# Optimization experiments

Measured on AMD Instinct MI355X. Metric: run time of the kernel, lower is better.

The kernel has to match this reference:

```python
import jax, jax.numpy as jnp
import numpy as np

N = 100000      # num_nodes
E = 1600000     # num_edges (avg degree 16)
D_IN = 128
D_H = 128
D_OUT = 128


def setup_inputs() -> dict:
    key = jax.random.key(0)
    ks = jax.random.split(key, 6)
    x = jax.random.normal(ks[0], (N, D_IN), dtype=jnp.float32)
    edge_index = jax.random.randint(ks[1], (2, E), 0, N, dtype=jnp.int32)
    s_in = 1.0 / np.sqrt(D_IN)
    s_h = 1.0 / np.sqrt(D_H)
    # nn.Linear weights have shape [out_features, in_features]
    w_neigh1 = jax.random.uniform(ks[2], (D_H, D_IN), jnp.float32, -s_in, s_in)
    w_root1 = jax.random.uniform(ks[3], (D_H, D_IN), jnp.float32, -s_in, s_in)
    w_neigh2 = jax.random.uniform(ks[4], (D_OUT, D_H), jnp.float32, -s_h, s_h)
    w_root2 = jax.random.uniform(ks[5], (D_OUT, D_H), jnp.float32, -s_h, s_h)
    return {
        "x": x,
        "w_neigh1": w_neigh1,
        "w_root1": w_root1,
        "w_neigh2": w_neigh2,
        "w_root2": w_root2,
        "edge_index": edge_index,
    }


def reference(x, w_neigh1, w_root1, w_neigh2, w_root2, edge_index):
    row = edge_index[0]  # destination (row of adjacency)
    col = edge_index[1]  # source / neighbor (column of adjacency)
    # row-normalized adjacency: adj[row, col] = 1 / deg(row)
    deg = jax.ops.segment_sum(jnp.ones(E, x.dtype), row, num_segments=N)
    inv_deg = jnp.where(deg > 0, 1.0 / jnp.maximum(deg, 1.0), 0.0)  # [N]

    def mean_agg(h):
        # spmm: gather neighbor feats [E, d], scatter-add to rows, normalize
        return jax.ops.segment_sum(h[col], row, num_segments=N) * inv_deg[:, None]

    # layer 0: relu(adj @ x @ Wn1^T + x @ Wr1^T)
    h = jax.nn.relu(mean_agg(x) @ w_neigh1.T + x @ w_root1.T)
    # layer 1: adj @ h @ Wn2^T + h @ Wr2^T
    return mean_agg(h) @ w_neigh2.T + h @ w_root2.T
```

## Files before the change

### kernel.cpp

```cpp
#include <hip/hip_runtime.h>

#define NBUK_MAX 2048
#define BNODE 64
#define BCAP 2048
#define AGG_NODES 16
#define AGG_CAP 768
#define SUPER_SHIFT 11
#define NSUPER_MAX 64
#define SCAP 65536
#define SUB_PER_SUPER 32

#define QSCALE (127.0f / 6.0f)
#define DEQ (6.0f / 127.0f)

typedef __attribute__((ext_vector_type(8))) short bf16x8;
typedef __attribute__((ext_vector_type(4))) float f32x4;

static __device__ __forceinline__ unsigned int f2bf(float f) {
  unsigned int t = __builtin_bit_cast(unsigned int, f);
  t += 0x7fff + ((t >> 16) & 1);
  return t >> 16;
}
static __device__ __forceinline__ unsigned char f2q(float v) {
  float q = rintf(v * QSCALE);
  q = fminf(fmaxf(q, -127.f), 127.f);
  return (unsigned char)(signed char)(int)q;
}



__global__ __launch_bounds__(256) void zero_kernel(int* __restrict__ p, int n) {
  int i = blockIdx.x * 256 + threadIdx.x;
  if (i < n) p[i] = 0;
}


__global__ __launch_bounds__(256) void prep_kernel(
    const float* __restrict__ x, unsigned short* __restrict__ Xp,
    unsigned char* __restrict__ Xq, const float* __restrict__ wn1,
    const float* __restrict__ wr1, const float* __restrict__ wn2,
    const float* __restrict__ wr2, unsigned short* __restrict__ Wp, int N,
    int cvtB) {
  const int b = blockIdx.x;
  const int tid = threadIdx.x;
  if (b < cvtB) {
    int i = b * 256 + tid;
    int n4 = N * 32;
    if (i < n4) {
      float4 v = ((const float4*)x)[i];
      unsigned int oq = (unsigned)f2q(v.x) | ((unsigned)f2q(v.y) << 8) |
                        ((unsigned)f2q(v.z) << 16) | ((unsigned)f2q(v.w) << 24);
      ((unsigned int*)Xq)[i] = oq;
      int r = i >> 5;
      int f0 = (i & 31) << 2;
      int tile = r >> 6, w = (r >> 4) & 3, m = r & 15;
      int ks = f0 >> 5, kgrp = (f0 >> 3) & 3, j0 = f0 & 7;
      unsigned dst =
          (unsigned)tile * 8192 + w * 2048 + ks * 512 + (kgrp * 16 + m) * 8 + j0;
      uint2 o;
      o.x = f2bf(v.x) | (f2bf(v.y) << 16);
      o.y = f2bf(v.z) | (f2bf(v.w) << 16);
      *(uint2*)(Xp + dst) = o;
    }
  } else {
    int i = (b - cvtB) * 256 + tid;
    int layer = i >> 15;
    int r = i & 32767;
    int ks = r >> 12;
    int nf = (r >> 9) & 7;
    int lane = (r >> 3) & 63;
    int j = r & 7;
    const float* src = layer ? ((ks < 4) ? wn2 : wr2) : ((ks < 4) ? wn1 : wr1);
    int m = lane & 15, kgrp = lane >> 4;
    int kk = (ks & 3) * 32 + kgrp * 8 + j;
    int n = nf * 16 + m;
    Wp[i] = (unsigned short)f2bf(src[n * 128 + kk]);
  }
}


__global__ __launch_bounds__(256) void s1_scatter(
    const int* __restrict__ row, const int* __restrict__ col,
    int* __restrict__ sfill, int* __restrict__ sbuf, int E) {
  __shared__ int cnt[NSUPER_MAX];
  __shared__ int base[NSUPER_MAX];
  int per = (E + gridDim.x - 1) / gridDim.x;
  int e0 = blockIdx.x * per;
  int e1 = e0 + per;
  if (e1 > E) e1 = E;
  if (threadIdx.x < NSUPER_MAX) cnt[threadIdx.x] = 0;
  __syncthreads();
  for (int e = e0 + threadIdx.x; e < e1; e += 256)
    atomicAdd(&cnt[row[e] >> SUPER_SHIFT], 1);
  __syncthreads();
  if (threadIdx.x < NSUPER_MAX) {
    int c = cnt[threadIdx.x];
    base[threadIdx.x] =
        c ? (threadIdx.x * SCAP + atomicAdd(&sfill[threadIdx.x], c)) : 0;
    cnt[threadIdx.x] = 0;
  }
  __syncthreads();
  for (int e = e0 + threadIdx.x; e < e1; e += 256) {
    int r = row[e];
    int sp = r >> SUPER_SHIFT;
    int rk = atomicAdd(&cnt[sp], 1);
    int w = base[sp] + rk;
    if (w < (sp + 1) * SCAP)
      sbuf[w] = ((r & ((1 << SUPER_SHIFT) - 1)) << 17) | col[e];
  }
}


__global__ __launch_bounds__(256) void s2_scatter(
    const int* __restrict__ sfillr, const int* __restrict__ sbuf,
    int* __restrict__ bfill, int* __restrict__ bbuf, int nbuk) {
  __shared__ int cnt[SUB_PER_SUPER];
  __shared__ int base[SUB_PER_SUPER];
  const int sp = blockIdx.x >> 4;
  const int bp = blockIdx.x & 15;
  const int b0 = sp * SUB_PER_SUPER;
  int scnt = sfillr[sp];
  if (scnt > SCAP) scnt = SCAP;
  const int sbase = sp * SCAP;
  const int i0 = sbase + (scnt * bp) / 16;
  const int i1 = sbase + (scnt * (bp + 1)) / 16;
  if (threadIdx.x < SUB_PER_SUPER) cnt[threadIdx.x] = 0;
  __syncthreads();
  for (int i = i0 + threadIdx.x; i < i1; i += 256)
    atomicAdd(&cnt[(((unsigned)sbuf[i]) >> 17) >> 6], 1);
  __syncthreads();
  if (threadIdx.x < SUB_PER_SUPER) {
    int c = cnt[threadIdx.x];
    int b = b0 + threadIdx.x;
    base[threadIdx.x] = c ? (b * BCAP + atomicAdd(&bfill[b], c)) : 0;
    cnt[threadIdx.x] = 0;
  }
  __syncthreads();
  for (int i = i0 + threadIdx.x; i < i1; i += 256) {
    int p = sbuf[i];
    unsigned rl = ((unsigned)p) >> 17;
    int sub = rl >> 6;
    int rk = atomicAdd(&cnt[sub], 1);
    int w = base[sub] + rk;
    if (w < (b0 + sub + 1) * BCAP)
      bbuf[w] = ((rl & 63) << 17) | (p & 0x1FFFF);
  }
}


__global__ __launch_bounds__(256) void p2_sort_kernel(
    const int* __restrict__ bfillr, int* __restrict__ bbuf,
    int* __restrict__ rowptr, int* __restrict__ bsz, int N) {
  __shared__ int cols[BCAP];
  __shared__ int hist[BNODE], startc[BNODE], fillc[BNODE];
  const int b = blockIdx.x;
  const int tid = threadIdx.x;
  const int gs = b * BCAP;
  int bsize = bfillr[b];
  if (bsize > BCAP) bsize = BCAP;
  if (tid < BNODE) hist[tid] = 0;
  __syncthreads();
  for (int i = tid; i < bsize; i += 256)
    atomicAdd(&hist[((unsigned)bbuf[gs + i]) >> 17], 1);
  __syncthreads();
  if (tid < 64) {
    int v = hist[tid];
    int s = v;
    #pragma unroll
    for (int off = 1; off < 64; off <<= 1) {
      int u = __shfl_up(s, off, 64);
      if (tid >= off) s += u;
    }
    startc[tid] = s - v;
    fillc[tid] = s - v;
  }
  __syncthreads();
  for (int i = tid; i < bsize; i += 256) {
    int p = bbuf[gs + i];
    int k = atomicAdd(&fillc[((unsigned)p) >> 17], 1);
    cols[k] = p & 0x1FFFF;
  }
  __syncthreads();
  for (int i = tid; i < bsize; i += 256) bbuf[gs + i] = cols[i];
  if (tid < BNODE) {
    int node = b * BNODE + tid;
    if (node <= N) rowptr[node] = gs + startc[tid];
  }
  if (tid == 0) bsz[b] = bsize;
}


__global__ __launch_bounds__(256) void agg_i8_kernel(
    const unsigned char* __restrict__ qtab, const int* __restrict__ rowptr,
    const int* __restrict__ bbuf, const int* __restrict__ bsz,
    unsigned short* __restrict__ outp, int N) {
  __shared__ int cols[AGG_CAP];
  __shared__ int rp[AGG_NODES + 1];
  const int tid = threadIdx.x;
  const int n0 = blockIdx.x * AGG_NODES;
  const int b = n0 >> 6;
  if (tid <= AGG_NODES) {
    int nn = n0 + tid;
    if (tid == AGG_NODES && (nn & 63) == 0) {
      rp[tid] = b * BCAP + bsz[b];
    } else {
      rp[tid] = rowptr[nn > N ? N : nn];
    }
  }
  __syncthreads();
  const int e0 = rp[0];
  const int range = rp[AGG_NODES] - e0;
  const bool lds = (range <= AGG_CAP);
  if (lds) {
    for (int i = tid; i < range; i += 256) cols[i] = bbuf[e0 + i];
  }
  __syncthreads();

  const int g = tid >> 4;
  const int fl = tid & 15;
  const int node = n0 + g;
  if (node >= N) return;
  const int d = rp[g + 1] - rp[g];
  const char* fb = (const char*)qtab;
  const unsigned foff = (unsigned)fl * 8;
  int a[8];
  #pragma unroll
  for (int j = 0; j < 8; ++j) a[j] = 0;

  const int* cp = lds ? (cols + (rp[g] - e0)) : (bbuf + rp[g]);
  for (int k0 = 0; k0 < d; k0 += 96) {
    int kend = d < k0 + 96 ? d : k0 + 96;
    unsigned sLoX = 0, sHiX = 0, sLoY = 0, sHiY = 0;
    int k = k0;
    for (; k + 8 <= kend; k += 8) {
      unsigned o[8];
      #pragma unroll
      for (int j = 0; j < 8; ++j) o[j] = ((unsigned)cp[k + j] << 7) + foff;
      uint2 v[8];
      #pragma unroll
      for (int j = 0; j < 8; ++j) v[j] = *(const uint2*)(fb + o[j]);
      #pragma unroll
      for (int j = 0; j < 8; ++j) {
        unsigned ux = v[j].x ^ 0x80808080u;
        unsigned uy = v[j].y ^ 0x80808080u;
        sLoX += ux & 0x00FF00FFu;
        sHiX += (ux >> 8) & 0x00FF00FFu;
        sLoY += uy & 0x00FF00FFu;
        sHiY += (uy >> 8) & 0x00FF00FFu;
      }
    }
    for (; k < kend; ++k) {
      uint2 v = *(const uint2*)(fb + (((unsigned)cp[k] << 7) + foff));
      unsigned ux = v.x ^ 0x80808080u;
      unsigned uy = v.y ^ 0x80808080u;
      sLoX += ux & 0x00FF00FFu;
      sHiX += (ux >> 8) & 0x00FF00FFu;
      sLoY += uy & 0x00FF00FFu;
      sHiY += (uy >> 8) & 0x00FF00FFu;
    }
    a[0] += (int)(sLoX & 0xFFFFu);
    a[2] += (int)(sLoX >> 16);
    a[1] += (int)(sHiX & 0xFFFFu);
    a[3] += (int)(sHiX >> 16);
    a[4] += (int)(sLoY & 0xFFFFu);
    a[6] += (int)(sLoY >> 16);
    a[5] += (int)(sHiY & 0xFFFFu);
    a[7] += (int)(sHiY >> 16);
  }
  const int bias = 128 * d;
  #pragma unroll
  for (int j = 0; j < 8; ++j) a[j] -= bias;

  float m = ((d > 0) ? 1.0f / (float)d : 0.f) * DEQ;
  uint4 pk;
  pk.x = f2bf((float)a[0] * m) | (f2bf((float)a[1] * m) << 16);
  pk.y = f2bf((float)a[2] * m) | (f2bf((float)a[3] * m) << 16);
  pk.z = f2bf((float)a[4] * m) | (f2bf((float)a[5] * m) << 16);
  pk.w = f2bf((float)a[6] * m) | (f2bf((float)a[7] * m) << 16);
  unsigned dst = ((unsigned)(node >> 6)) * 8192 + (((node >> 4) & 3) * 2048) +
                 ((fl >> 2) * 512) + (((fl & 3) * 16 + (node & 15)) * 8);
  *(uint4*)(outp + dst) = pk;
}


template <bool L1>
__global__ __launch_bounds__(256) void mfma_gemm_kernel(
    const unsigned short* __restrict__ Aagg_p,
    const unsigned short* __restrict__ Aroot_p,
    const unsigned short* __restrict__ Wpack,
    unsigned short* __restrict__ Hp, unsigned char* __restrict__ Hq,
    float* __restrict__ Cf, int nrows) {
  const int tid = threadIdx.x;
  const int lane = tid & 63;
  const int wid = tid >> 6;
  const int tile = blockIdx.x;
  const int n0 = tile * 64;
  const unsigned abase = (unsigned)tile * 8192 + wid * 2048 + lane * 8;

  bf16x8 a[8];
  #pragma unroll
  for (int ks = 0; ks < 4; ++ks)
    a[ks] = *(const bf16x8*)(Aagg_p + abase + ks * 512);
  #pragma unroll
  for (int ks = 0; ks < 4; ++ks)
    a[4 + ks] = *(const bf16x8*)(Aroot_p + abase + ks * 512);

  f32x4 acc[8];
  #pragma unroll
  for (int i = 0; i < 8; ++i) acc[i] = (f32x4){0.f, 0.f, 0.f, 0.f};
  const unsigned short* wp = Wpack + (size_t)lane * 8;
  #pragma unroll
  for (int ks = 0; ks < 8; ++ks) {
    #pragma unroll
    for (int nf = 0; nf < 8; ++nf) {
      bf16x8 bfr = *(const bf16x8*)(wp + ((ks * 8 + nf) << 9));
      acc[nf] = __builtin_amdgcn_mfma_f32_16x16x32_bf16(a[ks], bfr, acc[nf], 0, 0, 0);
    }
  }

  const int m = lane & 15;
  const int kgrp = lane >> 4;
  const int crow0 = n0 + (wid << 4) + kgrp * 4;
  #pragma unroll
  for (int nf = 0; nf < 8; ++nf) {
    int c = nf * 16 + m;
    #pragma unroll
    for (int j = 0; j < 4; ++j) {
      int r = crow0 + j;
      if (r < nrows) {
        float v = acc[nf][j];
        if (L1) {
          v = fmaxf(v, 0.f);
          unsigned dst = (unsigned)tile * 8192 + wid * 2048 + (c >> 5) * 512 +
                         ((((c >> 3) & 3) * 16) + (kgrp * 4 + j)) * 8 + (c & 7);
          Hp[dst] = (unsigned short)f2bf(v);
          Hq[(size_t)r * 128 + c] = f2q(v);
        } else {
          Cf[(size_t)r * 128 + c] = v;
        }
      }
    }
  }
}


extern "C" void kernel_launch(void* const* d_in, const int* in_sizes, int n_in,
                              void* d_out, int out_size, void* d_ws, size_t ws_size,
                              hipStream_t stream) {
  const float* x = (const float*)d_in[0];
  const float* wn1 = (const float*)d_in[1];
  const float* wr1 = (const float*)d_in[2];
  const float* wn2 = (const float*)d_in[3];
  const float* wr2 = (const float*)d_in[4];
  const int* ei = (const int*)d_in[5];
  const int N = in_sizes[0] / 128;
  const int E = in_sizes[5] / 2;
  const int* row = ei;
  const int* col = ei + E;
  const int NBUK = (N + BNODE - 1) / BNODE;
  const int NSUPER = (N + (1 << SUPER_SHIFT) - 1) >> SUPER_SHIFT;
  const size_t NT = (size_t)(N + 63) / 64;

  char* p = (char*)d_ws;
  unsigned short* Xp = (unsigned short*)p;  p += NT * 8192 * 2;
  unsigned short* Hp = (unsigned short*)p;  p += NT * 8192 * 2;
  unsigned short* Ap = (unsigned short*)p;  p += NT * 8192 * 2;
  unsigned char* Xq = (unsigned char*)p;    p += (size_t)N * 128;
  unsigned char* Hq = (unsigned char*)p;    p += (size_t)N * 128;
  int* sbuf = (int*)p;      p += (size_t)NSUPER_MAX * SCAP * 4;
  int* bbuf = (int*)p;      p += (size_t)NBUK_MAX * BCAP * 4;
  int* rowptr = (int*)p;    p += (size_t)(N + 1) * 4;
  int* sfill = (int*)p;     p += NSUPER_MAX * 4;
  int* bfill = (int*)p;     p += NBUK_MAX * 4;
  int* bsz = (int*)p;       p += NBUK_MAX * 4;
  unsigned short* Wp = (unsigned short*)p;  p += 2 * 32768 * 2;
  unsigned short* Wp1 = Wp;
  unsigned short* Wp2 = Wp + 32768;
  unsigned short* A2p = Xp;

  zero_kernel<<<(NSUPER_MAX + NBUK_MAX + 255) / 256, 256, 0, stream>>>(
      sfill, NSUPER_MAX + NBUK_MAX);

  int cvtB = (N * 32 + 255) / 256;
  prep_kernel<<<cvtB + 256, 256, 0, stream>>>(x, Xp, Xq, wn1, wr1, wn2, wr2, Wp,
                                              N, cvtB);

  s1_scatter<<<512, 256, 0, stream>>>(row, col, sfill, sbuf, E);
  s2_scatter<<<NSUPER * 16, 256, 0, stream>>>(sfill, sbuf, bfill, bbuf, NBUK);
  p2_sort_kernel<<<NBUK, 256, 0, stream>>>(bfill, bbuf, rowptr, bsz, N);

  agg_i8_kernel<<<(N + AGG_NODES - 1) / AGG_NODES, 256, 0, stream>>>(
      Xq, rowptr, bbuf, bsz, Ap, N);
  mfma_gemm_kernel<true><<<(int)NT, 256, 0, stream>>>(Ap, Xp, Wp1, Hp, Hq,
                                                      nullptr, N);

  agg_i8_kernel<<<(N + AGG_NODES - 1) / AGG_NODES, 256, 0, stream>>>(
      Hq, rowptr, bbuf, bsz, A2p, N);
  mfma_gemm_kernel<false><<<(int)NT, 256, 0, stream>>>(A2p, Hp, Wp2, nullptr,
                                                       nullptr, (float*)d_out, N);
}
```

Baseline: 179.3 us.

## Fuse edge scatter into prep kernel and split neighbor lists across lanes

The first-stage edge scatter now runs as extra blocks inside the input/weight conversion kernel, which removes one launch and lets the two independent jobs overlap. The int8 aggregation kernel now gives each 64-lane wavefront four nodes in turn. The four 16-lane slots split each node's neighbor list, and the partial sums are combined with cross-lane shuffles. This is meant to cut per-thread serial latency on long neighbor lists and balance load across degrees, at the cost of shuffle reductions and idle slots on low-degree nodes.

```diff
diff --git a/kernel.cpp b/kernel.cpp
--- a/kernel.cpp
+++ b/kernel.cpp
@@ -9,6 +9,7 @@
 #define NSUPER_MAX 64
 #define SCAP 65536
 #define SUB_PER_SUPER 32
+#define S1_BLOCKS 512
 
 #define QSCALE (127.0f / 6.0f)
 #define DEQ (6.0f / 127.0f)
@@ -39,8 +40,11 @@
     const float* __restrict__ x, unsigned short* __restrict__ Xp,
     unsigned char* __restrict__ Xq, const float* __restrict__ wn1,
     const float* __restrict__ wr1, const float* __restrict__ wn2,
-    const float* __restrict__ wr2, unsigned short* __restrict__ Wp, int N,
-    int cvtB) {
+    const float* __restrict__ wr2, unsigned short* __restrict__ Wp,
+    const int* __restrict__ row, const int* __restrict__ col,
+    int* __restrict__ sfill, int* __restrict__ sbuf, int N, int E, int cvtB) {
+  __shared__ int cnt[NSUPER_MAX];
+  __shared__ int base[NSUPER_MAX];
   const int b = blockIdx.x;
   const int tid = threadIdx.x;
   if (b < cvtB) {
@@ -62,7 +66,7 @@
       o.y = f2bf(v.z) | (f2bf(v.w) << 16);
       *(uint2*)(Xp + dst) = o;
     }
-  } else {
+  } else if (b < cvtB + 256) {
     int i = (b - cvtB) * 256 + tid;
     int layer = i >> 15;
     int r = i & 32767;
@@ -75,38 +79,31 @@
     int kk = (ks & 3) * 32 + kgrp * 8 + j;
     int n = nf * 16 + m;
     Wp[i] = (unsigned short)f2bf(src[n * 128 + kk]);
-  }
-}
-
-
-__global__ __launch_bounds__(256) void s1_scatter(
-    const int* __restrict__ row, const int* __restrict__ col,
-    int* __restrict__ sfill, int* __restrict__ sbuf, int E) {
-  __shared__ int cnt[NSUPER_MAX];
-  __shared__ int base[NSUPER_MAX];
-  int per = (E + gridDim.x - 1) / gridDim.x;
-  int e0 = blockIdx.x * per;
-  int e1 = e0 + per;
-  if (e1 > E) e1 = E;
-  if (threadIdx.x < NSUPER_MAX) cnt[threadIdx.x] = 0;
-  __syncthreads();
-  for (int e = e0 + threadIdx.x; e < e1; e += 256)
-    atomicAdd(&cnt[row[e] >> SUPER_SHIFT], 1);
-  __syncthreads();
-  if (threadIdx.x < NSUPER_MAX) {
-    int c = cnt[threadIdx.x];
-    base[threadIdx.x] =
-        c ? (threadIdx.x * SCAP + atomicAdd(&sfill[threadIdx.x], c)) : 0;
-    cnt[threadIdx.x] = 0;
-  }
-  __syncthreads();
-  for (int e = e0 + threadIdx.x; e < e1; e += 256) {
-    int r = row[e];
-    int sp = r >> SUPER_SHIFT;
-    int rk = atomicAdd(&cnt[sp], 1);
-    int w = base[sp] + rk;
-    if (w < (sp + 1) * SCAP)
-      sbuf[w] = ((r & ((1 << SUPER_SHIFT) - 1)) << 17) | col[e];
+  } else {
+    int hb = b - cvtB - 256;
+    int per = (E + S1_BLOCKS - 1) / S1_BLOCKS;
+    int e0 = hb * per;
+    int e1 = e0 + per;
+    if (e1 > E) e1 = E;
+    if (tid < NSUPER_MAX) cnt[tid] = 0;
+    __syncthreads();
+    for (int e = e0 + tid; e < e1; e += 256)
+      atomicAdd(&cnt[row[e] >> SUPER_SHIFT], 1);
+    __syncthreads();
+    if (tid < NSUPER_MAX) {
+      int c = cnt[tid];
+      base[tid] = c ? (tid * SCAP + atomicAdd(&sfill[tid], c)) : 0;
+      cnt[tid] = 0;
+    }
+    __syncthreads();
+    for (int e = e0 + tid; e < e1; e += 256) {
+      int r = row[e];
+      int sp = r >> SUPER_SHIFT;
+      int rk = atomicAdd(&cnt[sp], 1);
+      int w = base[sp] + rk;
+      if (w < (sp + 1) * SCAP)
+        sbuf[w] = ((r & ((1 << SUPER_SHIFT) - 1)) << 17) | col[e];
+    }
   }
 }
 
@@ -216,70 +213,82 @@
   }
   __syncthreads();
 
-  const int g = tid >> 4;
-  const int fl = tid & 15;
-  const int node = n0 + g;
-  if (node >= N) return;
-  const int d = rp[g + 1] - rp[g];
+  const int wv = tid >> 6;
+  const int lane = tid & 63;
+  const int slot = lane >> 4;
+  const int fl = lane & 15;
   const char* fb = (const char*)qtab;
   const unsigned foff = (unsigned)fl * 8;
-  int a[8];
-  #pragma unroll
-  for (int j = 0; j < 8; ++j) a[j] = 0;
-
-  const int* cp = lds ? (cols + (rp[g] - e0)) : (bbuf + rp[g]);
-  for (int k0 = 0; k0 < d; k0 += 96) {
-    int kend = d < k0 + 96 ? d : k0 + 96;
-    unsigned sLoX = 0, sHiX = 0, sLoY = 0, sHiY = 0;
-    int k = k0;
-    for (; k + 8 <= kend; k += 8) {
-      unsigned o[8];
-      #pragma unroll
-      for (int j = 0; j < 8; ++j) o[j] = ((unsigned)cp[k + j] << 7) + foff;
-      uint2 v[8];
-      #pragma unroll
-      for (int j = 0; j < 8; ++j) v[j] = *(const uint2*)(fb + o[j]);
-      #pragma unroll
-      for (int j = 0; j < 8; ++j) {
-        unsigned ux = v[j].x ^ 0x80808080u;
-        unsigned uy = v[j].y ^ 0x80808080u;
+
+  #pragma unroll
+  for (int q = 0; q < 4; ++q) {
+    const int nl = wv * 4 + q;
+    const int node = n0 + nl;
+    if (node >= N) continue;
+    const int d = rp[nl + 1] - rp[nl];
+    const int* cp = lds ? (cols + (rp[nl] - e0)) : (bbuf + rp[nl]);
+    int a[8];
+    #pragma unroll
+    for (int j = 0; j < 8; ++j) a[j] = 0;
+
+    for (int k0 = 0; k0 < d; k0 += 64) {
+      const int kend = d < k0 + 64 ? d : k0 + 64;
+      unsigned sLoX = 0, sHiX = 0, sLoY = 0, sHiY = 0;
+      int k = k0;
+      for (; k + 16 <= kend; k += 16) {
+        unsigned o[4];
+        #pragma unroll
+        for (int j = 0; j < 4; ++j)
+          o[j] = ((unsigned)cp[k + slot + j * 4] << 7) + foff;
+        uint2 v[4];
+        #pragma unroll
+        for (int j = 0; j < 4; ++j) v[j] = *(const uint2*)(fb + o[j]);
+        #pragma unroll
+        for (int j = 0; j < 4; ++j) {
+          unsigned ux = v[j].x ^ 0x80808080u;
+          unsigned uy = v[j].y ^ 0x80808080u;
+          sLoX += ux & 0x00FF00FFu;
+          sHiX += (ux >> 8) & 0x00FF00FFu;
+          sLoY += uy & 0x00FF00FFu;
+          sHiY += (uy >> 8) & 0x00FF00FFu;
+        }
+      }
+      for (int kk = k + slot; kk < kend; kk += 4) {
+        uint2 v = *(const uint2*)(fb + (((unsigned)cp[kk] << 7) + foff));
+        unsigned ux = v.x ^ 0x80808080u;
+        unsigned uy = v.y ^ 0x80808080u;
         sLoX += ux & 0x00FF00FFu;
         sHiX += (ux >> 8) & 0x00FF00FFu;
         sLoY += uy & 0x00FF00FFu;
         sHiY += (uy >> 8) & 0x00FF00FFu;
       }
-    }
-    for (; k < kend; ++k) {
-      uint2 v = *(const uint2*)(fb + (((unsigned)cp[k] << 7) + foff));
-      unsigned ux = v.x ^ 0x80808080u;
-      unsigned uy = v.y ^ 0x80808080u;
-      sLoX += ux & 0x00FF00FFu;
-      sHiX += (ux >> 8) & 0x00FF00FFu;
-      sLoY += uy & 0x00FF00FFu;
-      sHiY += (uy >> 8) & 0x00FF00FFu;
-    }
-    a[0] += (int)(sLoX & 0xFFFFu);
-    a[2] += (int)(sLoX >> 16);
-    a[1] += (int)(sHiX & 0xFFFFu);
-    a[3] += (int)(sHiX >> 16);
-    a[4] += (int)(sLoY & 0xFFFFu);
-    a[6] += (int)(sLoY >> 16);
-    a[5] += (int)(sHiY & 0xFFFFu);
-    a[7] += (int)(sHiY >> 16);
-  }
-  const int bias = 128 * d;
-  #pragma unroll
-  for (int j = 0; j < 8; ++j) a[j] -= bias;
-
-  float m = ((d > 0) ? 1.0f / (float)d : 0.f) * DEQ;
-  uint4 pk;
-  pk.x = f2bf((float)a[0] * m) | (f2bf((float)a[1] * m) << 16);
-  pk.y = f2bf((float)a[2] * m) | (f2bf((float)a[3] * m) << 16);
-  pk.z = f2bf((float)a[4] * m) | (f2bf((float)a[5] * m) << 16);
-  pk.w = f2bf((float)a[6] * m) | (f2bf((float)a[7] * m) << 16);
-  unsigned dst = ((unsigned)(node >> 6)) * 8192 + (((node >> 4) & 3) * 2048) +
-                 ((fl >> 2) * 512) + (((fl & 3) * 16 + (node & 15)) * 8);
-  *(uint4*)(outp + dst) = pk;
+      a[0] += (int)(sLoX & 0xFFFFu);
+      a[2] += (int)(sLoX >> 16);
+      a[1] += (int)(sHiX & 0xFFFFu);
+      a[3] += (int)(sHiX >> 16);
+      a[4] += (int)(sLoY & 0xFFFFu);
+      a[6] += (int)(sLoY >> 16);
+      a[5] += (int)(sHiY & 0xFFFFu);
+      a[7] += (int)(sHiY >> 16);
+    }
+    #pragma unroll
+    for (int j = 0; j < 8; ++j) {
+      a[j] += __shfl_xor(a[j], 16, 64);
+      a[j] += __shfl_xor(a[j], 32, 64);
+    }
+    if (slot == 0) {
+      const int bias = 128 * d;
+      float m = ((d > 0) ? 1.0f / (float)d : 0.f) * DEQ;
+      uint4 pk;
+      pk.x = f2bf((float)(a[0] - bias) * m) | (f2bf((float)(a[1] - bias) * m) << 16);
+      pk.y = f2bf((float)(a[2] - bias) * m) | (f2bf((float)(a[3] - bias) * m) << 16);
+      pk.z = f2bf((float)(a[4] - bias) * m) | (f2bf((float)(a[5] - bias) * m) << 16);
+      pk.w = f2bf((float)(a[6] - bias) * m) | (f2bf((float)(a[7] - bias) * m) << 16);
+      unsigned dst = ((unsigned)(node >> 6)) * 8192 + (((node >> 4) & 3) * 2048) +
+                     ((fl >> 2) * 512) + (((fl & 3) * 16 + (node & 15)) * 8);
+      *(uint4*)(outp + dst) = pk;
+    }
+  }
 }
 
 
@@ -382,10 +391,9 @@
       sfill, NSUPER_MAX + NBUK_MAX);
 
   int cvtB = (N * 32 + 255) / 256;
-  prep_kernel<<<cvtB + 256, 256, 0, stream>>>(x, Xp, Xq, wn1, wr1, wn2, wr2, Wp,
-                                              N, cvtB);
-
-  s1_scatter<<<512, 256, 0, stream>>>(row, col, sfill, sbuf, E);
+  prep_kernel<<<cvtB + 256 + S1_BLOCKS, 256, 0, stream>>>(
+      x, Xp, Xq, wn1, wr1, wn2, wr2, Wp, row, col, sfill, sbuf, N, E, cvtB);
+
   s2_scatter<<<NSUPER * 16, 256, 0, stream>>>(sfill, sbuf, bfill, bbuf, NBUK);
   p2_sort_kernel<<<NBUK, 256, 0, stream>>>(bfill, bbuf, rowptr, bsz, N);
 
```

Measured after the change: 201.9 us. 12.6% more time.
